# Performance work log

Measured on AMD Instinct MI355X. Metric: run time of the kernel, lower is better.

The kernel has to match this reference:

```python
import jax, jax.numpy as jnp
import numpy as np

B, T, S = 32, 64, 64
V, E, H, Hs = 32000, 512, 512, 512
D2 = 2 * Hs  # src feature dim


def setup_inputs() -> dict:
    key = jax.random.key(0)
    ks = jax.random.split(key, 26)
    n = lambda k, shape, s=0.05: (jax.random.normal(k, shape, jnp.float32) * s)
    inp = {
        'src': jax.random.normal(ks[0], (B, S, D2), jnp.float32),
        'trg': jax.random.randint(ks[1], (B, T), 0, V),
        'mask': jnp.ones((B, T), jnp.float32),
        'emb': n(ks[2], (V, E)),
        # PyTorch LSTMCell params: weight_ih [4H, E+H], weight_hh [4H, H]
        'f_Wih': n(ks[3], (4 * H, E + H)), 'f_Whh': n(ks[4], (4 * H, H)),
        'f_bih': n(ks[5], (4 * H,)), 'f_bhh': n(ks[6], (4 * H,)),
        'b_Wih': n(ks[7], (4 * H, E + H)), 'b_Whh': n(ks[8], (4 * H, H)),
        'b_bih': n(ks[9], (4 * H,)), 'b_bhh': n(ks[10], (4 * H,)),
        # attention projections: hidden -> 2*src_hidden
        'fatt_W': n(ks[11], (D2, H)), 'fatt_b': n(ks[12], (D2,)),
        'batt_W': n(ks[13], (D2, H)), 'batt_b': n(ks[14], (D2,)),
        # att_hidden linears: (H + 2*Hs) -> H
        'fah_W': n(ks[15], (H, H + D2)), 'fah_b': n(ks[16], (H,)),
        'bah_W': n(ks[17], (H, H + D2)), 'bah_b': n(ks[18], (H,)),
        # output projection 2H -> V
        'fc_W': n(ks[19], (V, 2 * H)), 'fc_b': n(ks[20], (V,)),
        'feed_init': n(ks[21], (2 * H,), 1.0),
        'hid_init': n(ks[22], (4 * H,), 1.0),
    }
    return inp


def reference(src, trg, mask, emb, f_Wih, f_Whh, f_bih, f_bhh,
              b_Wih, b_Whh, b_bih, b_bhh, fatt_W, fatt_b, batt_W, batt_b,
              fah_W, fah_b, bah_W, bah_b, fc_W, fc_b, feed_init, hid_init):
    Bn = src.shape[0]
    Hn = feed_init.shape[0] // 2
    scale = 1.0 / np.sqrt(Hn)  # key.size(-1) == trg hidden before projection

    x = emb[trg]  # [B, T, E]  (dropout p=0 -> identity)

    hhat0 = jnp.broadcast_to(feed_init, (Bn, 2 * Hn))
    f_hhat0, b_hhat0 = jnp.split(hhat0, 2, axis=1)
    hid0 = jnp.broadcast_to(hid_init, (Bn, 4 * Hn))
    f_hid, b_hid = jnp.split(hid0, 2, axis=-1)
    f_h0, f_c0 = jnp.split(f_hid, 2, axis=-1)
    b_h0, b_c0 = jnp.split(b_hid, 2, axis=-1)

    def lstm(xin, h, c, Wih, Whh, bih, bhh):
        g = xin @ Wih.T + bih + h @ Whh.T + bhh
        i, f, gg, o = jnp.split(g, 4, axis=-1)
        c = jax.nn.sigmoid(f) * c + jax.nn.sigmoid(i) * jnp.tanh(gg)
        h = jax.nn.sigmoid(o) * jnp.tanh(c)
        return h, c

    def att(h, W, b):
        k = h @ W.T + b                              # [B, 2Hs]
        w = jnp.einsum('bd,bsd->bs', k, src) * scale  # [B, S]
        p = jax.nn.softmax(w, axis=-1)
        return jnp.einsum('bs,bsd->bd', p, src)       # [B, 2Hs]

    xs = jnp.swapaxes(x, 0, 1)      # [T, B, E]
    ms = jnp.swapaxes(mask, 0, 1)   # [T, B]

    def f_step(carry, x_t):
        h, c, hhat = carry
        h, c = lstm(jnp.concatenate([x_t, hhat], -1), h, c, f_Wih, f_Whh, f_bih, f_bhh)
        ct = att(h, fatt_W, fatt_b)
        # NOTE: original uses b_att_hidden in the forward loop (faithful)
        hhat = jnp.tanh(jnp.concatenate([h, ct], -1) @ bah_W.T + bah_b)
        return (h, c, hhat), hhat

    _, f_out = jax.lax.scan(f_step, (f_h0, f_c0, f_hhat0), xs)  # [T, B, H]

    def b_step(carry, inp):
        x_t, m_t = inp
        h, c, hhat = carry
        hn, cn = lstm(jnp.concatenate([x_t, hhat], -1), h, c, b_Wih, b_Whh, b_bih, b_bhh)
        h = m_t[:, None] * hn
        c = m_t[:, None] * cn
        ct = att(h, batt_W, batt_b)
        # NOTE: original uses f_att_hidden in the backward loop (faithful)
        hhat = jnp.tanh(jnp.concatenate([h, ct], -1) @ fah_W.T + fah_b)
        return (h, c, hhat), hhat

    _, b_out = jax.lax.scan(b_step, (b_h0, b_c0, b_hhat0), (xs[::-1], ms[::-1]))

    f_out = jnp.swapaxes(f_out, 0, 1)        # [B, T, H]
    b_cheat = jnp.swapaxes(b_out, 0, 1)      # reversed-time order, as stacked in torch
    # b_outputs[:, :-2] = b_outputs_cheat[:, 2:]; last two steps zero (faithful)
    b_shift = jnp.concatenate([b_cheat[:, 2:], jnp.zeros_like(b_cheat[:, :2])], axis=1)

    logits = jnp.concatenate([f_out, b_shift], -1) @ fc_W.T + fc_b  # [B, T, V]
    return logits
```

## Files before the change

kernel.cpp:

```cpp
#include <hip/hip_runtime.h>
#include <hip/hip_bf16.h>
#include <math.h>

typedef __hip_bfloat16 bf16;
typedef __attribute__((ext_vector_type(8))) short short8b;
typedef __attribute__((ext_vector_type(8))) __bf16 bf16x8;
typedef __attribute__((ext_vector_type(4))) float f32x4;

#define SCALE_F 0.04419417382415922f

template <typename V>
static __device__ inline auto mfma_try(V a, V b, f32x4 c, int)
    -> decltype(__builtin_amdgcn_mfma_f32_16x16x32_bf16(a, b, c, 0, 0, 0)) {
  return __builtin_amdgcn_mfma_f32_16x16x32_bf16(a, b, c, 0, 0, 0);
}
template <typename V>
static __device__ inline auto mfma_try(V a, V b, f32x4 c, long)
    -> decltype(__builtin_amdgcn_mfma_f32_16x16x32_bf16(
        __builtin_bit_cast(bf16x8, a), __builtin_bit_cast(bf16x8, b), c, 0, 0, 0)) {
  return __builtin_amdgcn_mfma_f32_16x16x32_bf16(
      __builtin_bit_cast(bf16x8, a), __builtin_bit_cast(bf16x8, b), c, 0, 0, 0);
}
static __device__ inline f32x4 MFMA(short8b a, short8b b, f32x4 c) {
  return mfma_try(a, b, c, 0);
}

static __device__ inline short8b ldb8(const bf16* p) {
  return *reinterpret_cast<const short8b*>(p);
}
static __device__ inline float b2f(bf16 v) { return __bfloat162float(v); }
static __device__ inline bf16 f2b(float v) { return __float2bfloat16(v); }
static __device__ inline float s2f(short s) {
  unsigned u = ((unsigned)(unsigned short)s) << 16;
  return __builtin_bit_cast(float, u);
}
static __device__ inline float sigm(float x) { return 1.f / (1.f + expf(-x)); }

static __device__ inline void st2_wt(bf16* p, float v) {
  unsigned short u = __builtin_bit_cast(unsigned short, f2b(v));
  unsigned ud = u;
  asm volatile("global_store_short %0, %1, off sc0 sc1" ::"v"(p), "v"(ud)
               : "memory");
}

static __device__ inline void st_flag(unsigned* p, unsigned v) {
  asm volatile("global_store_dword %0, %1, off sc0 sc1" ::"v"(p), "v"(v)
               : "memory");
}
static __device__ inline unsigned ld_flag(const unsigned* p) {
  unsigned v;
  asm volatile("global_load_dword %0, %1, off sc0 sc1\n\ts_waitcnt vmcnt(0)"
               : "=v"(v)
               : "v"(p)
               : "memory");
  return v;
}

static __device__ inline void gbar(unsigned* flags, unsigned ep, int blk, int tid) {
  asm volatile("s_waitcnt vmcnt(0)" ::: "memory");
  __syncthreads();
  if (tid < 64) {
    unsigned* row = flags + (size_t)ep * 64;
    if (tid == 0) st_flag(row + blk, 1u);
    while (true) {
      const unsigned v = ld_flag(row + tid);
      if (__ballot(v != 0) == ~0ull) break;
      __builtin_amdgcn_s_sleep(1);
    }
  }
  __syncthreads();
}

template <typename OutT, bool HAS_BIAS>
__global__ __launch_bounds__(256) void gemm_k(
    const bf16* __restrict__ A, const bf16* __restrict__ Bw,
    OutT* __restrict__ C, const float* __restrict__ bias,
    int M, int N, int K) {
  const int lane = threadIdx.x & 63;
  const int wid = threadIdx.x >> 6;
  const int m0 = blockIdx.y * 128 + (wid >> 1) * 64;
  const int n0 = blockIdx.x * 128 + (wid & 1) * 64;
  const int lr = lane & 15;
  const int lk = (lane >> 4) * 8;
  f32x4 acc[4][4];
#pragma unroll
  for (int i = 0; i < 4; ++i)
#pragma unroll
    for (int j = 0; j < 4; ++j) acc[i][j] = (f32x4){0.f, 0.f, 0.f, 0.f};
  const bf16* Ap = A + (size_t)(m0 + lr) * K + lk;
  const bf16* Bp = Bw + (size_t)(n0 + lr) * K + lk;
  for (int k0 = 0; k0 < K; k0 += 32) {
    short8b av[4], bv[4];
#pragma unroll
    for (int i = 0; i < 4; ++i) av[i] = ldb8(Ap + (size_t)i * 16 * K + k0);
#pragma unroll
    for (int i = 0; i < 4; ++i) bv[i] = ldb8(Bp + (size_t)i * 16 * K + k0);
#pragma unroll
    for (int mi = 0; mi < 4; ++mi)
#pragma unroll
      for (int ni = 0; ni < 4; ++ni)
        acc[mi][ni] = MFMA(av[mi], bv[ni], acc[mi][ni]);
  }
  const int rb = (lane >> 4) * 4;
#pragma unroll
  for (int mi = 0; mi < 4; ++mi) {
#pragma unroll
    for (int r = 0; r < 4; ++r) {
      const int row = m0 + mi * 16 + rb + r;
#pragma unroll
      for (int ni = 0; ni < 4; ++ni) {
        const int col = n0 + ni * 16 + lr;
        float v = acc[mi][ni][r];
        if (HAS_BIAS) v += bias[col];
        if constexpr (sizeof(OutT) == 2) {
          C[(size_t)row * N + col] = f2b(v);
        } else {
          C[(size_t)row * N + col] = v;
        }
      }
    }
  }
}

__global__ void k_xg(const float* __restrict__ emb, const int* __restrict__ trg,
                     bf16* __restrict__ xg) {
  const int i = blockIdx.x * 256 + threadIdx.x;
  const int r = i >> 9, e = i & 511;
  const int t = r >> 5, b = r & 31;
  const int tok = trg[b * 64 + t];
  xg[i] = f2b(emb[(size_t)tok * 512 + e]);
}

__global__ void k_srcb(const float* __restrict__ s, bf16* __restrict__ d) {
  const int i = blockIdx.x * 256 + threadIdx.x;
  d[i] = f2b(s[i]);
}

__global__ void k_fcw(const float* __restrict__ s, bf16* __restrict__ d) {
  const size_t stride = (size_t)gridDim.x * blockDim.x;
  for (size_t i = blockIdx.x * (size_t)blockDim.x + threadIdx.x;
       i < (size_t)32000 * 1024; i += stride)
    d[i] = f2b(s[i]);
}

__global__ void k_wpack(const float* __restrict__ fWih, const float* __restrict__ fWhh,
                        const float* __restrict__ bWih, const float* __restrict__ bWhh,
                        const float* __restrict__ fattW, const float* __restrict__ battW,
                        const float* __restrict__ bahW, const float* __restrict__ fahW,
                        bf16* Wxf, bf16* Wxb, bf16* Wrecf, bf16* Wrecb,
                        bf16* attWtf, bf16* attWtb, bf16* ahW2f, bf16* ahW2b,
                        bf16* Wh1f, bf16* Wh1b) {
  const int stride = gridDim.x * blockDim.x;
  const int i0 = blockIdx.x * blockDim.x + threadIdx.x;
  for (int i = i0; i < 2048 * 512; i += stride) {
    const int gc = i >> 9, k = i & 511;
    Wxf[i] = f2b(fWih[(size_t)gc * 1024 + k]);
    Wxb[i] = f2b(bWih[(size_t)gc * 1024 + k]);
  }
  for (int i = i0; i < 2048 * 1024; i += stride) {
    const int gc = i >> 10, k = i & 1023;
    float vf, vb;
    if (k < 512) { vf = fWih[(size_t)gc * 1024 + 512 + k]; vb = bWih[(size_t)gc * 1024 + 512 + k]; }
    else         { vf = fWhh[(size_t)gc * 512 + k - 512]; vb = bWhh[(size_t)gc * 512 + k - 512]; }
    Wrecf[i] = f2b(vf); Wrecb[i] = f2b(vb);
  }
  for (int i = i0; i < 512 * 1024; i += stride) {
    const int j = i >> 10, d = i & 1023;
    attWtf[i] = f2b(fattW[(size_t)d * 512 + j]);
    attWtb[i] = f2b(battW[(size_t)d * 512 + j]);
  }
  for (int i = i0; i < 512 * 1024; i += stride) {
    const int o = i >> 10, d = i & 1023;
    ahW2f[i] = f2b(bahW[(size_t)o * 1536 + 512 + d]);
    ahW2b[i] = f2b(fahW[(size_t)o * 1536 + 512 + d]);
  }
  for (int i = i0; i < 512 * 512; i += stride) {
    const int o = i >> 9, k = i & 511;
    Wh1f[i] = f2b(bahW[(size_t)o * 1536 + k]);
    Wh1b[i] = f2b(fahW[(size_t)o * 1536 + k]);
  }
}

__global__ void k_c0(const float* __restrict__ src, const float* __restrict__ fb,
                     const float* __restrict__ bb, float* __restrict__ c0f,
                     float* __restrict__ c0b) {
  const int r = blockIdx.x;
  const int tid = threadIdx.x;
  float pf = 0.f, pb = 0.f;
  for (int d = tid; d < 1024; d += 256) {
    const float s = src[(size_t)r * 1024 + d];
    pf += s * fb[d];
    pb += s * bb[d];
  }
#pragma unroll
  for (int d = 1; d < 64; d <<= 1) { pf += __shfl_xor(pf, d); pb += __shfl_xor(pb, d); }
  __shared__ float rf[4], rb2[4];
  if ((tid & 63) == 0) { rf[tid >> 6] = pf; rb2[tid >> 6] = pb; }
  __syncthreads();
  if (tid == 0) {
    c0f[r] = (rf[0] + rf[1] + rf[2] + rf[3]) * SCALE_F;
    c0b[r] = (rb2[0] + rb2[1] + rb2[2] + rb2[3]) * SCALE_F;
  }
}

__global__ void k_init(const float* __restrict__ feed, const float* __restrict__ hid,
                       bf16* hh0, bf16* hh1, bf16* hb0, bf16* hb1,
                       float* cst0, float* cst1) {
  const int i = blockIdx.x * 256 + threadIdx.x;
  const int b = i >> 9, k = i & 511;
  hh0[i] = f2b(feed[k]);
  hh1[i] = f2b(feed[512 + k]);
  hb0[i] = f2b(hid[k]);
  hb1[i] = f2b(hid[1024 + k]);
  cst0[k * 32 + b] = hid[512 + k];
  cst1[k * 32 + b] = hid[1536 + k];
}

struct ScanP {
  const bf16* Wrec[2]; const bf16* Xp[2]; const bf16* Af[2]; const bf16* Bm[2];
  const bf16* Wh1[2]; const float* bih[2]; const float* bhh[2];
  const float* c0[2]; const float* ahb[2]; const float* mask;
  bf16* hh[2]; bf16* hb[2]; bf16* U[2]; float* cst[2]; bf16* hcat; unsigned* flags;
};

__global__ __launch_bounds__(256) void scan_k(ScanP P) {
  const int blk = blockIdx.x;
  const int dir = blk >> 5;
  const int g = blk & 31;
  const int tid = threadIdx.x;
  const int lane = tid & 63;
  const int wv = tid >> 6;

  const bf16* __restrict__ Wrec = P.Wrec[dir];
  const bf16* __restrict__ Xp = P.Xp[dir];
  const bf16* __restrict__ Af = P.Af[dir];
  const bf16* __restrict__ Bm = P.Bm[dir];
  const bf16* __restrict__ Wh1 = P.Wh1[dir];
  const float* __restrict__ bihp = P.bih[dir];
  const float* __restrict__ bhhp = P.bhh[dir];
  const float* __restrict__ c0v = P.c0[dir];
  const float* __restrict__ ahbp = P.ahb[dir];
  bf16* __restrict__ hhB = P.hh[dir];
  bf16* __restrict__ hbB = P.hb[dir];
  bf16* __restrict__ Ubuf = P.U[dir];
  float* __restrict__ cst = P.cst[dir];

  __shared__ float gl[4][16][33];
  __shared__ float h_lds[512];
  __shared__ float w_part[2][64];
  __shared__ float p_lds[64];

  unsigned ep = 0;
  const int lr16 = lane & 15;
  const int koff = (lane >> 4) * 8;

  short8b pA0[16], pA1[16];
  {
    const bf16* A0 = hbB + (size_t)lr16 * 512;
    const bf16* A1 = hbB + (size_t)(lr16 + 16) * 512;
#pragma unroll
    for (int ks = 0; ks < 16; ++ks) {
      pA0[ks] = ldb8(A0 + ks * 32 + koff);
      pA1[ks] = ldb8(A1 + ks * 32 + koff);
    }
  }

  for (int t = 0; t < 64; ++t) {
    const bf16* hhR = hhB + (size_t)t * 32 * 512;
    bf16* hhW = hhB + (size_t)(t + 1) * 32 * 512;
    bf16* hbW = hbB + (size_t)(t + 1) * 32 * 512;

    {
      const int gate = wv;
      const int gc = gate * 512 + g * 16 + lr16;
      const bf16* Brow = Wrec + (size_t)gc * 1024;
      const bf16* A0h = hhR + (size_t)lr16 * 512;
      const bf16* A1h = hhR + (size_t)(lr16 + 16) * 512;
      f32x4 ac0 = (f32x4){0.f, 0.f, 0.f, 0.f};
      f32x4 ac1 = (f32x4){0.f, 0.f, 0.f, 0.f};
#pragma unroll
      for (int ks = 0; ks < 16; ++ks) {
        const int k = ks * 32 + koff;
        const short8b bv = ldb8(Brow + 512 + k);
        ac0 = MFMA(pA0[ks], bv, ac0);
        ac1 = MFMA(pA1[ks], bv, ac1);
      }
#pragma unroll
      for (int ks = 0; ks < 16; ++ks) {
        const int k = ks * 32 + koff;
        const short8b bv = ldb8(Brow + k);
        ac0 = MFMA(ldb8(A0h + k), bv, ac0);
        ac1 = MFMA(ldb8(A1h + k), bv, ac1);
      }
      const int tcol = dir ? (63 - t) : t;
      const float bsum = bihp[gc] + bhhp[gc];
      const bf16* xpc = Xp + (size_t)gc * 2048 + tcol * 32;
#pragma unroll
      for (int r = 0; r < 4; ++r) {
        const int brow = (lane >> 4) * 4 + r;
        gl[gate][lr16][brow] = ac0[r] + b2f(xpc[brow]) + bsum;
        gl[gate][lr16][brow + 16] = ac1[r] + b2f(xpc[brow + 16]) + bsum;
      }
    }
    __syncthreads();
    {
      const int b = tid & 31;
#pragma unroll
      for (int it = 0; it < 2; ++it) {
        const int jl = (tid >> 5) + it * 8;
        const int j = g * 16 + jl;
        const float gi = gl[0][jl][b];
        const float gf = gl[1][jl][b];
        const float gg = gl[2][jl][b];
        const float go = gl[3][jl][b];
        float cn = sigm(gf) * cst[j * 32 + b] + sigm(gi) * tanhf(gg);
        float hn = sigm(go) * tanhf(cn);
        if (dir) {
          const float m = P.mask[b * 64 + (63 - t)];
          hn *= m; cn *= m;
        }
        cst[j * 32 + b] = cn;
        st2_wt(hbW + (size_t)b * 512 + j, hn);
      }
    }
    gbar(P.flags, ep++, blk, tid);

    if (wv == 0) {
      const bf16* Brow = Wh1 + (size_t)(g * 16 + lr16) * 512;
      const bf16* A0 = hbW + (size_t)lr16 * 512;
      const bf16* A1 = hbW + (size_t)(lr16 + 16) * 512;
      f32x4 u0 = (f32x4){0.f, 0.f, 0.f, 0.f};
      f32x4 u1 = (f32x4){0.f, 0.f, 0.f, 0.f};
#pragma unroll
      for (int ks = 0; ks < 16; ++ks) {
        const int k = ks * 32 + koff;
        const short8b bv = ldb8(Brow + k);
        u0 = MFMA(ldb8(A0 + k), bv, u0);
        u1 = MFMA(ldb8(A1 + k), bv, u1);
      }
      bf16* Uw = Ubuf + (size_t)t * 32 * 512;
      const int o = g * 16 + lr16;
#pragma unroll
      for (int r = 0; r < 4; ++r) {
        const int b0 = (lane >> 4) * 4 + r;
        st2_wt(Uw + (size_t)b0 * 512 + o, u0[r]);
        st2_wt(Uw + (size_t)(b0 + 16) * 512 + o, u1[r]);
      }
    } else if (wv == 1) {
      const short8b v = ldb8(hbW + (size_t)g * 512 + lane * 8);
#pragma unroll
      for (int e = 0; e < 8; ++e) h_lds[lane * 8 + e] = s2f(v[e]);
    }
    __syncthreads();
    if (wv == 1 || wv == 2) {
      const int s = lane, q = wv - 1;
      const bf16* arow = Af + (size_t)(g * 64 + s) * 512 + q * 256;
      float part = 0.f;
#pragma unroll 4
      for (int k8 = 0; k8 < 256; k8 += 8) {
        const short8b v = ldb8(arow + k8);
#pragma unroll
        for (int e = 0; e < 8; ++e) part += h_lds[q * 256 + k8 + e] * s2f(v[e]);
      }
      w_part[q][s] = part;
    }
    __syncthreads();
    if (wv == 3) {
      const float v = (w_part[0][lane] + w_part[1][lane]) * SCALE_F + c0v[g * 64 + lane];
      float mx = v;
#pragma unroll
      for (int d = 1; d < 64; d <<= 1) mx = fmaxf(mx, __shfl_xor(mx, d));
      const float e = expf(v - mx);
      float sm = e;
#pragma unroll
      for (int d = 1; d < 64; d <<= 1) sm += __shfl_xor(sm, d);
      p_lds[lane] = e / sm;
    }
    __syncthreads();
    float a2[2];
#pragma unroll
    for (int it = 0; it < 2; ++it) {
      const int o = tid + it * 256;
      float acc = ahbp[o];
      const bf16* bmc = Bm + (size_t)(g * 64) * 512 + o;
#pragma unroll 4
      for (int s2 = 0; s2 < 64; ++s2) acc += p_lds[s2] * b2f(bmc[(size_t)s2 * 512]);
      a2[it] = acc;
    }
    gbar(P.flags, ep++, blk, tid);

    {
      const bf16* Ur = Ubuf + ((size_t)t * 32 + g) * 512;
#pragma unroll
      for (int it = 0; it < 2; ++it) {
        const int o = tid + it * 256;
        const float hh = tanhf(a2[it] + b2f(Ur[o]));
        st2_wt(hhW + (size_t)g * 512 + o, hh);
        if (dir == 0) {
          P.hcat[(size_t)(g * 64 + t) * 1024 + o] = f2b(hh);
        } else if (t >= 2) {
          P.hcat[(size_t)(g * 64 + t - 2) * 1024 + 512 + o] = f2b(hh);
        }
      }
      if (t < 63) {
        const bf16* A0 = hbW + (size_t)lr16 * 512;
        const bf16* A1 = hbW + (size_t)(lr16 + 16) * 512;
#pragma unroll
        for (int ks = 0; ks < 16; ++ks) {
          pA0[ks] = ldb8(A0 + ks * 32 + koff);
          pA1[ks] = ldb8(A1 + ks * 32 + koff);
        }
      }
    }
    gbar(P.flags, ep++, blk, tid);
  }
}

extern "C" void kernel_launch(void* const* d_in, const int* in_sizes, int n_in,
                              void* d_out, int out_size, void* d_ws, size_t ws_size,
                              hipStream_t stream) {
  (void)in_sizes; (void)n_in; (void)out_size; (void)ws_size;
  const float* src  = (const float*)d_in[0];
  const int*   trg  = (const int*)d_in[1];
  const float* mask = (const float*)d_in[2];
  const float* emb  = (const float*)d_in[3];
  const float* fWih = (const float*)d_in[4];
  const float* fWhh = (const float*)d_in[5];
  const float* fbih = (const float*)d_in[6];
  const float* fbhh = (const float*)d_in[7];
  const float* bWih = (const float*)d_in[8];
  const float* bWhh = (const float*)d_in[9];
  const float* bbih = (const float*)d_in[10];
  const float* bbhh = (const float*)d_in[11];
  const float* fattW = (const float*)d_in[12];
  const float* fattb = (const float*)d_in[13];
  const float* battW = (const float*)d_in[14];
  const float* battb = (const float*)d_in[15];
  const float* fahW = (const float*)d_in[16];
  const float* fahb = (const float*)d_in[17];
  const float* bahW = (const float*)d_in[18];
  const float* bahb = (const float*)d_in[19];
  const float* fcW  = (const float*)d_in[20];
  const float* fcb  = (const float*)d_in[21];
  const float* feed = (const float*)d_in[22];
  const float* hid  = (const float*)d_in[23];

  char* wsp = (char*)d_ws;
  size_t off = 0;
  auto alloc = [&](size_t bytes) -> void* {
    void* p = wsp + off;
    off += (bytes + 255) & ~(size_t)255;
    return p;
  };
  unsigned* flags = (unsigned*)alloc((size_t)192 * 64 * 4);
  bf16* hcat = (bf16*)alloc((size_t)2048 * 1024 * 2);
  const size_t zero_bytes = off;
  bf16* xg    = (bf16*)alloc((size_t)2048 * 512 * 2);
  bf16* srcb  = (bf16*)alloc((size_t)2048 * 1024 * 2);
  bf16* fcWb  = (bf16*)alloc((size_t)32000 * 1024 * 2);
  bf16* Wxf   = (bf16*)alloc((size_t)2048 * 512 * 2);
  bf16* Wxb   = (bf16*)alloc((size_t)2048 * 512 * 2);
  bf16* Wrecf = (bf16*)alloc((size_t)2048 * 1024 * 2);
  bf16* Wrecb = (bf16*)alloc((size_t)2048 * 1024 * 2);
  bf16* attWtf = (bf16*)alloc((size_t)512 * 1024 * 2);
  bf16* attWtb = (bf16*)alloc((size_t)512 * 1024 * 2);
  bf16* ahW2f = (bf16*)alloc((size_t)512 * 1024 * 2);
  bf16* ahW2b = (bf16*)alloc((size_t)512 * 1024 * 2);
  bf16* Wh1f  = (bf16*)alloc((size_t)512 * 512 * 2);
  bf16* Wh1b  = (bf16*)alloc((size_t)512 * 512 * 2);
  bf16* Xpf   = (bf16*)alloc((size_t)2048 * 2048 * 2);
  bf16* Xpb   = (bf16*)alloc((size_t)2048 * 2048 * 2);
  bf16* Aff   = (bf16*)alloc((size_t)2048 * 512 * 2);
  bf16* Afb   = (bf16*)alloc((size_t)2048 * 512 * 2);
  bf16* Bmf   = (bf16*)alloc((size_t)2048 * 512 * 2);
  bf16* Bmb   = (bf16*)alloc((size_t)2048 * 512 * 2);
  float* c0f  = (float*)alloc(2048 * 4);
  float* c0b  = (float*)alloc(2048 * 4);
  bf16* hh0   = (bf16*)alloc((size_t)65 * 32 * 512 * 2);
  bf16* hh1   = (bf16*)alloc((size_t)65 * 32 * 512 * 2);
  bf16* hb0   = (bf16*)alloc((size_t)65 * 32 * 512 * 2);
  bf16* hb1   = (bf16*)alloc((size_t)65 * 32 * 512 * 2);
  bf16* Uf    = (bf16*)alloc((size_t)64 * 32 * 512 * 2);
  bf16* Ub    = (bf16*)alloc((size_t)64 * 32 * 512 * 2);
  float* cst0 = (float*)alloc((size_t)512 * 32 * 4);
  float* cst1 = (float*)alloc((size_t)512 * 32 * 4);

  hipMemsetAsync(d_ws, 0, zero_bytes, stream);

  k_xg<<<4096, 256, 0, stream>>>(emb, trg, xg);
  k_srcb<<<8192, 256, 0, stream>>>(src, srcb);
  k_fcw<<<8192, 256, 0, stream>>>(fcW, fcWb);
  k_wpack<<<2048, 256, 0, stream>>>(fWih, fWhh, bWih, bWhh, fattW, battW, bahW, fahW,
                                    Wxf, Wxb, Wrecf, Wrecb, attWtf, attWtb, ahW2f, ahW2b,
                                    Wh1f, Wh1b);
  k_c0<<<2048, 256, 0, stream>>>(src, fattb, battb, c0f, c0b);
  k_init<<<64, 256, 0, stream>>>(feed, hid, hh0, hh1, hb0, hb1, cst0, cst1);

  gemm_k<bf16, false><<<dim3(16, 16), 256, 0, stream>>>(Wxf, xg, Xpf, nullptr, 2048, 2048, 512);
  gemm_k<bf16, false><<<dim3(16, 16), 256, 0, stream>>>(Wxb, xg, Xpb, nullptr, 2048, 2048, 512);
  gemm_k<bf16, false><<<dim3(4, 16), 256, 0, stream>>>(srcb, attWtf, Aff, nullptr, 2048, 512, 1024);
  gemm_k<bf16, false><<<dim3(4, 16), 256, 0, stream>>>(srcb, attWtb, Afb, nullptr, 2048, 512, 1024);
  gemm_k<bf16, false><<<dim3(4, 16), 256, 0, stream>>>(srcb, ahW2f, Bmf, nullptr, 2048, 512, 1024);
  gemm_k<bf16, false><<<dim3(4, 16), 256, 0, stream>>>(srcb, ahW2b, Bmb, nullptr, 2048, 512, 1024);

  ScanP sp;
  sp.Wrec[0] = Wrecf; sp.Wrec[1] = Wrecb;
  sp.Xp[0] = Xpf;     sp.Xp[1] = Xpb;
  sp.Af[0] = Aff;     sp.Af[1] = Afb;
  sp.Bm[0] = Bmf;     sp.Bm[1] = Bmb;
  sp.Wh1[0] = Wh1f;   sp.Wh1[1] = Wh1b;
  sp.bih[0] = fbih;   sp.bih[1] = bbih;
  sp.bhh[0] = fbhh;   sp.bhh[1] = bbhh;
  sp.c0[0] = c0f;     sp.c0[1] = c0b;
  sp.ahb[0] = bahb;   sp.ahb[1] = fahb;
  sp.mask = mask;
  sp.hh[0] = hh0;     sp.hh[1] = hh1;
  sp.hb[0] = hb0;     sp.hb[1] = hb1;
  sp.U[0] = Uf;       sp.U[1] = Ub;
  sp.cst[0] = cst0;   sp.cst[1] = cst1;
  sp.hcat = hcat;     sp.flags = flags;
  scan_k<<<64, 256, 0, stream>>>(sp);

  gemm_k<float, true><<<dim3(250, 16), 256, 0, stream>>>(hcat, fcWb, (float*)d_out, fcb,
                                                         2048, 32000, 1024);
}
```

Before: 2.940 ms.

## Consolidate scan into 16 large blocks with per-direction 8-block grid barriers

The recurrent scan kernel now runs as 16 blocks of 1024 threads, each packing four former 256-thread groups, instead of 64 blocks of 256. Grid barriers are split per direction and wait on only 8 flags, which cuts the number of participants in each cross-block sync. The kernel also drops the register-cached hb operand in favour of reloading it each step, and it packs bf16 stores into dword writes. The trade-off is fewer CUs doing the per-step work and more register and LDS pressure per block.

```diff
diff --git a/kernel.cpp b/kernel.cpp
--- a/kernel.cpp
+++ b/kernel.cpp
@@ -34,12 +34,21 @@
   unsigned u = ((unsigned)(unsigned short)s) << 16;
   return __builtin_bit_cast(float, u);
 }
+static __device__ inline unsigned pack2(float lo, float hi) {
+  const unsigned a = (unsigned)__builtin_bit_cast(unsigned short, f2b(lo));
+  const unsigned b = (unsigned)__builtin_bit_cast(unsigned short, f2b(hi));
+  return a | (b << 16);
+}
 static __device__ inline float sigm(float x) { return 1.f / (1.f + expf(-x)); }
 
 static __device__ inline void st2_wt(bf16* p, float v) {
-  unsigned short u = __builtin_bit_cast(unsigned short, f2b(v));
-  unsigned ud = u;
+  unsigned ud = (unsigned)__builtin_bit_cast(unsigned short, f2b(v));
   asm volatile("global_store_short %0, %1, off sc0 sc1" ::"v"(p), "v"(ud)
+               : "memory");
+}
+static __device__ inline void st4_wt(bf16* p, float lo, float hi) {
+  unsigned ud = pack2(lo, hi);
+  asm volatile("global_store_dword %0, %1, off sc0 sc1" ::"v"(p), "v"(ud)
                : "memory");
 }
 
@@ -56,14 +65,14 @@
   return v;
 }
 
-static __device__ inline void gbar(unsigned* flags, unsigned ep, int blk, int tid) {
+static __device__ inline void gbar8(unsigned* flg, unsigned ep, int bd, int tid) {
   asm volatile("s_waitcnt vmcnt(0)" ::: "memory");
   __syncthreads();
   if (tid < 64) {
-    unsigned* row = flags + (size_t)ep * 64;
-    if (tid == 0) st_flag(row + blk, 1u);
+    unsigned* row = flg + (size_t)ep * 64;
+    if (tid == 0) st_flag(row + bd, 1u);
     while (true) {
-      const unsigned v = ld_flag(row + tid);
+      const unsigned v = ld_flag(row + (tid & 7));
       if (__ballot(v != 0) == ~0ull) break;
       __builtin_amdgcn_s_sleep(1);
     }
@@ -223,13 +232,15 @@
   bf16* hh[2]; bf16* hb[2]; bf16* U[2]; float* cst[2]; bf16* hcat; unsigned* flags;
 };
 
-__global__ __launch_bounds__(256) void scan_k(ScanP P) {
+__global__ __launch_bounds__(1024) void scan_k(ScanP P) {
   const int blk = blockIdx.x;
-  const int dir = blk >> 5;
-  const int g = blk & 31;
+  const int dir = blk >> 3;
+  const int bd = blk & 7;
   const int tid = threadIdx.x;
   const int lane = tid & 63;
   const int wv = tid >> 6;
+  const int grp = wv >> 2;
+  const int sub = wv & 3;
 
   const bf16* __restrict__ Wrec = P.Wrec[dir];
   const bf16* __restrict__ Xp = P.Xp[dir];
@@ -244,88 +255,81 @@
   bf16* __restrict__ hbB = P.hb[dir];
   bf16* __restrict__ Ubuf = P.U[dir];
   float* __restrict__ cst = P.cst[dir];
-
-  __shared__ float gl[4][16][33];
-  __shared__ float h_lds[512];
-  __shared__ float w_part[2][64];
-  __shared__ float p_lds[64];
+  unsigned* __restrict__ flg = P.flags + (size_t)dir * 192 * 64;
+
+  __shared__ float gl[4][4][16][33];
+  __shared__ float h_lds[4][512];
+  __shared__ float w_part[4][2][64];
+  __shared__ float p_lds[4][64];
 
   unsigned ep = 0;
   const int lr16 = lane & 15;
-  const int koff = (lane >> 4) * 8;
-
-  short8b pA0[16], pA1[16];
-  {
-    const bf16* A0 = hbB + (size_t)lr16 * 512;
-    const bf16* A1 = hbB + (size_t)(lr16 + 16) * 512;
-#pragma unroll
-    for (int ks = 0; ks < 16; ++ks) {
-      pA0[ks] = ldb8(A0 + ks * 32 + koff);
-      pA1[ks] = ldb8(A1 + ks * 32 + koff);
-    }
-  }
+  const int kb = lane >> 4;
+  const int koff = kb * 8;
+  const int g = bd * 4 + grp;
 
   for (int t = 0; t < 64; ++t) {
     const bf16* hhR = hhB + (size_t)t * 32 * 512;
     bf16* hhW = hhB + (size_t)(t + 1) * 32 * 512;
+    const bf16* hbR = hbB + (size_t)t * 32 * 512;
     bf16* hbW = hbB + (size_t)(t + 1) * 32 * 512;
 
     {
-      const int gate = wv;
+      const int gate = sub;
       const int gc = gate * 512 + g * 16 + lr16;
       const bf16* Brow = Wrec + (size_t)gc * 1024;
       const bf16* A0h = hhR + (size_t)lr16 * 512;
       const bf16* A1h = hhR + (size_t)(lr16 + 16) * 512;
+      const bf16* A0g = hbR + (size_t)lr16 * 512;
+      const bf16* A1g = hbR + (size_t)(lr16 + 16) * 512;
       f32x4 ac0 = (f32x4){0.f, 0.f, 0.f, 0.f};
       f32x4 ac1 = (f32x4){0.f, 0.f, 0.f, 0.f};
 #pragma unroll
       for (int ks = 0; ks < 16; ++ks) {
         const int k = ks * 32 + koff;
-        const short8b bv = ldb8(Brow + 512 + k);
-        ac0 = MFMA(pA0[ks], bv, ac0);
-        ac1 = MFMA(pA1[ks], bv, ac1);
-      }
-#pragma unroll
-      for (int ks = 0; ks < 16; ++ks) {
-        const int k = ks * 32 + koff;
-        const short8b bv = ldb8(Brow + k);
-        ac0 = MFMA(ldb8(A0h + k), bv, ac0);
-        ac1 = MFMA(ldb8(A1h + k), bv, ac1);
+        const short8b bh = ldb8(Brow + 512 + k);
+        ac0 = MFMA(ldb8(A0g + k), bh, ac0);
+        ac1 = MFMA(ldb8(A1g + k), bh, ac1);
+        const short8b bx = ldb8(Brow + k);
+        ac0 = MFMA(ldb8(A0h + k), bx, ac0);
+        ac1 = MFMA(ldb8(A1h + k), bx, ac1);
       }
       const int tcol = dir ? (63 - t) : t;
       const float bsum = bihp[gc] + bhhp[gc];
       const bf16* xpc = Xp + (size_t)gc * 2048 + tcol * 32;
 #pragma unroll
       for (int r = 0; r < 4; ++r) {
-        const int brow = (lane >> 4) * 4 + r;
-        gl[gate][lr16][brow] = ac0[r] + b2f(xpc[brow]) + bsum;
-        gl[gate][lr16][brow + 16] = ac1[r] + b2f(xpc[brow + 16]) + bsum;
+        const int brow = kb * 4 + r;
+        gl[gate][grp][lr16][brow] = ac0[r] + b2f(xpc[brow]) + bsum;
+        gl[gate][grp][lr16][brow + 16] = ac1[r] + b2f(xpc[brow + 16]) + bsum;
       }
     }
     __syncthreads();
     {
-      const int b = tid & 31;
-#pragma unroll
-      for (int it = 0; it < 2; ++it) {
-        const int jl = (tid >> 5) + it * 8;
-        const int j = g * 16 + jl;
-        const float gi = gl[0][jl][b];
-        const float gf = gl[1][jl][b];
-        const float gg = gl[2][jl][b];
-        const float go = gl[3][jl][b];
+      const int b = tid >> 5;
+      const int j2 = tid & 31;
+      const float m = dir ? P.mask[b * 64 + (63 - t)] : 1.f;
+      float hn2[2];
+#pragma unroll
+      for (int u = 0; u < 2; ++u) {
+        const int jl = j2 * 2 + u;
+        const int jq = jl >> 4, jr = jl & 15;
+        const float gi = gl[0][jq][jr][b];
+        const float gf = gl[1][jq][jr][b];
+        const float gg = gl[2][jq][jr][b];
+        const float go = gl[3][jq][jr][b];
+        const int j = bd * 64 + jl;
         float cn = sigm(gf) * cst[j * 32 + b] + sigm(gi) * tanhf(gg);
         float hn = sigm(go) * tanhf(cn);
-        if (dir) {
-          const float m = P.mask[b * 64 + (63 - t)];
-          hn *= m; cn *= m;
-        }
+        hn *= m; cn *= m;
         cst[j * 32 + b] = cn;
-        st2_wt(hbW + (size_t)b * 512 + j, hn);
-      }
-    }
-    gbar(P.flags, ep++, blk, tid);
-
-    if (wv == 0) {
+        hn2[u] = hn;
+      }
+      st4_wt(hbW + (size_t)b * 512 + bd * 64 + j2 * 2, hn2[0], hn2[1]);
+    }
+    gbar8(flg, ep++, bd, tid);
+
+    if (sub == 0) {
       const bf16* Brow = Wh1 + (size_t)(g * 16 + lr16) * 512;
       const bf16* A0 = hbW + (size_t)lr16 * 512;
       const bf16* A1 = hbW + (size_t)(lr16 + 16) * 512;
@@ -342,31 +346,32 @@
       const int o = g * 16 + lr16;
 #pragma unroll
       for (int r = 0; r < 4; ++r) {
-        const int b0 = (lane >> 4) * 4 + r;
+        const int b0 = kb * 4 + r;
         st2_wt(Uw + (size_t)b0 * 512 + o, u0[r]);
         st2_wt(Uw + (size_t)(b0 + 16) * 512 + o, u1[r]);
       }
-    } else if (wv == 1) {
+    } else if (sub == 1) {
       const short8b v = ldb8(hbW + (size_t)g * 512 + lane * 8);
 #pragma unroll
-      for (int e = 0; e < 8; ++e) h_lds[lane * 8 + e] = s2f(v[e]);
+      for (int e = 0; e < 8; ++e) h_lds[grp][lane * 8 + e] = s2f(v[e]);
     }
     __syncthreads();
-    if (wv == 1 || wv == 2) {
-      const int s = lane, q = wv - 1;
-      const bf16* arow = Af + (size_t)(g * 64 + s) * 512 + q * 256;
+    if (sub == 1 || sub == 2) {
+      const int q = sub - 1;
+      const bf16* arow = Af + (size_t)(g * 64 + lane) * 512 + q * 256;
       float part = 0.f;
 #pragma unroll 4
       for (int k8 = 0; k8 < 256; k8 += 8) {
         const short8b v = ldb8(arow + k8);
 #pragma unroll
-        for (int e = 0; e < 8; ++e) part += h_lds[q * 256 + k8 + e] * s2f(v[e]);
-      }
-      w_part[q][s] = part;
+        for (int e = 0; e < 8; ++e) part += h_lds[grp][q * 256 + k8 + e] * s2f(v[e]);
+      }
+      w_part[grp][q][lane] = part;
     }
     __syncthreads();
-    if (wv == 3) {
-      const float v = (w_part[0][lane] + w_part[1][lane]) * SCALE_F + c0v[g * 64 + lane];
+    if (sub == 3) {
+      const float v = (w_part[grp][0][lane] + w_part[grp][1][lane]) * SCALE_F +
+                      c0v[g * 64 + lane];
       float mx = v;
 #pragma unroll
       for (int d = 1; d < 64; d <<= 1) mx = fmaxf(mx, __shfl_xor(mx, d));
@@ -374,45 +379,42 @@
       float sm = e;
 #pragma unroll
       for (int d = 1; d < 64; d <<= 1) sm += __shfl_xor(sm, d);
-      p_lds[lane] = e / sm;
+      p_lds[grp][lane] = e / sm;
     }
     __syncthreads();
     float a2[2];
-#pragma unroll
-    for (int it = 0; it < 2; ++it) {
-      const int o = tid + it * 256;
-      float acc = ahbp[o];
-      const bf16* bmc = Bm + (size_t)(g * 64) * 512 + o;
+    {
+      const int tg = sub * 64 + lane;
+      const int o2 = tg * 2;
+      a2[0] = ahbp[o2];
+      a2[1] = ahbp[o2 + 1];
+      const bf16* bmc = Bm + (size_t)(g * 64) * 512 + o2;
 #pragma unroll 4
-      for (int s2 = 0; s2 < 64; ++s2) acc += p_lds[s2] * b2f(bmc[(size_t)s2 * 512]);
-      a2[it] = acc;
-    }
-    gbar(P.flags, ep++, blk, tid);
+      for (int s2 = 0; s2 < 64; ++s2) {
+        const unsigned uv = *reinterpret_cast<const unsigned*>(bmc + (size_t)s2 * 512);
+        const float p = p_lds[grp][s2];
+        a2[0] += p * s2f((short)(uv & 0xffffu));
+        a2[1] += p * s2f((short)(uv >> 16));
+      }
+    }
+    gbar8(flg, ep++, bd, tid);
 
     {
-      const bf16* Ur = Ubuf + ((size_t)t * 32 + g) * 512;
-#pragma unroll
-      for (int it = 0; it < 2; ++it) {
-        const int o = tid + it * 256;
-        const float hh = tanhf(a2[it] + b2f(Ur[o]));
-        st2_wt(hhW + (size_t)g * 512 + o, hh);
-        if (dir == 0) {
-          P.hcat[(size_t)(g * 64 + t) * 1024 + o] = f2b(hh);
-        } else if (t >= 2) {
-          P.hcat[(size_t)(g * 64 + t - 2) * 1024 + 512 + o] = f2b(hh);
-        }
-      }
-      if (t < 63) {
-        const bf16* A0 = hbW + (size_t)lr16 * 512;
-        const bf16* A1 = hbW + (size_t)(lr16 + 16) * 512;
-#pragma unroll
-        for (int ks = 0; ks < 16; ++ks) {
-          pA0[ks] = ldb8(A0 + ks * 32 + koff);
-          pA1[ks] = ldb8(A1 + ks * 32 + koff);
-        }
-      }
-    }
-    gbar(P.flags, ep++, blk, tid);
+      const int tg = sub * 64 + lane;
+      const int o2 = tg * 2;
+      const unsigned uu =
+          *reinterpret_cast<const unsigned*>(Ubuf + ((size_t)t * 32 + g) * 512 + o2);
+      const float h0 = tanhf(a2[0] + s2f((short)(uu & 0xffffu)));
+      const float h1 = tanhf(a2[1] + s2f((short)(uu >> 16)));
+      st4_wt(hhW + (size_t)g * 512 + o2, h0, h1);
+      const unsigned hp = pack2(h0, h1);
+      if (dir == 0) {
+        *reinterpret_cast<unsigned*>(P.hcat + (size_t)(g * 64 + t) * 1024 + o2) = hp;
+      } else if (t >= 2) {
+        *reinterpret_cast<unsigned*>(P.hcat + (size_t)(g * 64 + t - 2) * 1024 + 512 + o2) = hp;
+      }
+    }
+    gbar8(flg, ep++, bd, tid);
   }
 }
 
@@ -452,7 +454,7 @@
     off += (bytes + 255) & ~(size_t)255;
     return p;
   };
-  unsigned* flags = (unsigned*)alloc((size_t)192 * 64 * 4);
+  unsigned* flags = (unsigned*)alloc((size_t)2 * 192 * 64 * 4);
   bf16* hcat = (bf16*)alloc((size_t)2048 * 1024 * 2);
   const size_t zero_bytes = off;
   bf16* xg    = (bf16*)alloc((size_t)2048 * 512 * 2);
@@ -519,7 +521,7 @@
   sp.U[0] = Uf;       sp.U[1] = Ub;
   sp.cst[0] = cst0;   sp.cst[1] = cst1;
   sp.hcat = hcat;     sp.flags = flags;
-  scan_k<<<64, 256, 0, stream>>>(sp);
+  scan_k<<<16, 1024, 0, stream>>>(sp);
 
   gemm_k<float, true><<<dim3(250, 16), 256, 0, stream>>>(hcat, fcWb, (float*)d_out, fcb,
                                                          2048, 32000, 1024);
```

Result: slower. 5.093 ms (+73.2%).

## Pin each scan direction to one XCC and use per-direction barriers

Applied to the files above, without the earlier changes.

The scan kernel now launches many blocks and reads the hardware XCC id. Blocks on XCC 0 and 1 claim ranks through atomics, so each direction's 32 workgroups share one XCC and its L2, and all other blocks exit. The global barrier is split per direction over 32 groups, and the write-through sc0/sc1 stores of the shared h/U buffers become plain stores, relying on same-XCC L2 coherence. This targets cross-XCC synchronisation and coherence cost in the recurrent loop, but it depends on the hardware dispatching enough blocks to each XCC, adds a bounded spin guard that can fall through silently, and it adds a tiny launch of many exiting blocks.

```diff
diff --git a/kernel.cpp b/kernel.cpp
--- a/kernel.cpp
+++ b/kernel.cpp
@@ -34,13 +34,16 @@
   unsigned u = ((unsigned)(unsigned short)s) << 16;
   return __builtin_bit_cast(float, u);
 }
+static __device__ inline unsigned pack2(float lo, float hi) {
+  const unsigned a = (unsigned)__builtin_bit_cast(unsigned short, f2b(lo));
+  const unsigned b = (unsigned)__builtin_bit_cast(unsigned short, f2b(hi));
+  return a | (b << 16);
+}
 static __device__ inline float sigm(float x) { return 1.f / (1.f + expf(-x)); }
 
-static __device__ inline void st2_wt(bf16* p, float v) {
-  unsigned short u = __builtin_bit_cast(unsigned short, f2b(v));
-  unsigned ud = u;
-  asm volatile("global_store_short %0, %1, off sc0 sc1" ::"v"(p), "v"(ud)
-               : "memory");
+static __device__ inline void st2p(bf16* p, float v) { *p = f2b(v); }
+static __device__ inline void st4p(bf16* p, float lo, float hi) {
+  *reinterpret_cast<unsigned*>(p) = pack2(lo, hi);
 }
 
 static __device__ inline void st_flag(unsigned* p, unsigned v) {
@@ -56,14 +59,15 @@
   return v;
 }
 
-static __device__ inline void gbar(unsigned* flags, unsigned ep, int blk, int tid) {
+static __device__ inline void xbar(unsigned* flg, unsigned ep, int g, int tid) {
   asm volatile("s_waitcnt vmcnt(0)" ::: "memory");
   __syncthreads();
   if (tid < 64) {
-    unsigned* row = flags + (size_t)ep * 64;
-    if (tid == 0) st_flag(row + blk, 1u);
-    while (true) {
-      const unsigned v = ld_flag(row + tid);
+    unsigned* row = flg + (size_t)ep * 64;
+    if (tid == 0) st_flag(row + g, 1u);
+    int guard = 0;
+    while (guard++ < (1 << 22)) {
+      const unsigned v = ld_flag(row + (tid & 31));
       if (__ballot(v != 0) == ~0ull) break;
       __builtin_amdgcn_s_sleep(1);
     }
@@ -220,13 +224,26 @@
   const bf16* Wrec[2]; const bf16* Xp[2]; const bf16* Af[2]; const bf16* Bm[2];
   const bf16* Wh1[2]; const float* bih[2]; const float* bhh[2];
   const float* c0[2]; const float* ahb[2]; const float* mask;
-  bf16* hh[2]; bf16* hb[2]; bf16* U[2]; float* cst[2]; bf16* hcat; unsigned* flags;
+  bf16* hh[2]; bf16* hb[2]; bf16* U[2]; float* cst[2]; bf16* hcat;
+  unsigned* flags; unsigned* claim;
 };
 
 __global__ __launch_bounds__(256) void scan_k(ScanP P) {
-  const int blk = blockIdx.x;
-  const int dir = blk >> 5;
-  const int g = blk & 31;
+  __shared__ int s_dir, s_g;
+  if (threadIdx.x == 0) {
+    unsigned xcc;
+    asm volatile("s_getreg_b32 %0, hwreg(HW_REG_XCC_ID)" : "=s"(xcc));
+    xcc &= 7u;
+    int rank = 1000;
+    if (xcc < 2) rank = (int)atomicAdd(P.claim + xcc, 1u);
+    s_dir = (int)xcc;
+    s_g = rank;
+  }
+  __syncthreads();
+  const int dir = s_dir;
+  const int g = s_g;
+  if (dir >= 2 || g >= 32) return;
+
   const int tid = threadIdx.x;
   const int lane = tid & 63;
   const int wv = tid >> 6;
@@ -244,6 +261,7 @@
   bf16* __restrict__ hbB = P.hb[dir];
   bf16* __restrict__ Ubuf = P.U[dir];
   float* __restrict__ cst = P.cst[dir];
+  unsigned* __restrict__ flg = P.flags + (size_t)dir * 192 * 64;
 
   __shared__ float gl[4][16][33];
   __shared__ float h_lds[512];
@@ -252,7 +270,8 @@
 
   unsigned ep = 0;
   const int lr16 = lane & 15;
-  const int koff = (lane >> 4) * 8;
+  const int kb = lane >> 4;
+  const int koff = kb * 8;
 
   short8b pA0[16], pA1[16];
   {
@@ -297,7 +316,7 @@
       const bf16* xpc = Xp + (size_t)gc * 2048 + tcol * 32;
 #pragma unroll
       for (int r = 0; r < 4; ++r) {
-        const int brow = (lane >> 4) * 4 + r;
+        const int brow = kb * 4 + r;
         gl[gate][lr16][brow] = ac0[r] + b2f(xpc[brow]) + bsum;
         gl[gate][lr16][brow + 16] = ac1[r] + b2f(xpc[brow + 16]) + bsum;
       }
@@ -320,10 +339,10 @@
           hn *= m; cn *= m;
         }
         cst[j * 32 + b] = cn;
-        st2_wt(hbW + (size_t)b * 512 + j, hn);
-      }
-    }
-    gbar(P.flags, ep++, blk, tid);
+        st2p(hbW + (size_t)b * 512 + j, hn);
+      }
+    }
+    xbar(flg, ep++, g, tid);
 
     if (wv == 0) {
       const bf16* Brow = Wh1 + (size_t)(g * 16 + lr16) * 512;
@@ -342,9 +361,9 @@
       const int o = g * 16 + lr16;
 #pragma unroll
       for (int r = 0; r < 4; ++r) {
-        const int b0 = (lane >> 4) * 4 + r;
-        st2_wt(Uw + (size_t)b0 * 512 + o, u0[r]);
-        st2_wt(Uw + (size_t)(b0 + 16) * 512 + o, u1[r]);
+        const int b0 = kb * 4 + r;
+        st2p(Uw + (size_t)b0 * 512 + o, u0[r]);
+        st2p(Uw + (size_t)(b0 + 16) * 512 + o, u1[r]);
       }
     } else if (wv == 1) {
       const short8b v = ldb8(hbW + (size_t)g * 512 + lane * 8);
@@ -353,8 +372,8 @@
     }
     __syncthreads();
     if (wv == 1 || wv == 2) {
-      const int s = lane, q = wv - 1;
-      const bf16* arow = Af + (size_t)(g * 64 + s) * 512 + q * 256;
+      const int q = wv - 1;
+      const bf16* arow = Af + (size_t)(g * 64 + lane) * 512 + q * 256;
       float part = 0.f;
 #pragma unroll 4
       for (int k8 = 0; k8 < 256; k8 += 8) {
@@ -362,7 +381,7 @@
 #pragma unroll
         for (int e = 0; e < 8; ++e) part += h_lds[q * 256 + k8 + e] * s2f(v[e]);
       }
-      w_part[q][s] = part;
+      w_part[q][lane] = part;
     }
     __syncthreads();
     if (wv == 3) {
@@ -387,7 +406,7 @@
       for (int s2 = 0; s2 < 64; ++s2) acc += p_lds[s2] * b2f(bmc[(size_t)s2 * 512]);
       a2[it] = acc;
     }
-    gbar(P.flags, ep++, blk, tid);
+    xbar(flg, ep++, g, tid);
 
     {
       const bf16* Ur = Ubuf + ((size_t)t * 32 + g) * 512;
@@ -395,7 +414,7 @@
       for (int it = 0; it < 2; ++it) {
         const int o = tid + it * 256;
         const float hh = tanhf(a2[it] + b2f(Ur[o]));
-        st2_wt(hhW + (size_t)g * 512 + o, hh);
+        st2p(hhW + (size_t)g * 512 + o, hh);
         if (dir == 0) {
           P.hcat[(size_t)(g * 64 + t) * 1024 + o] = f2b(hh);
         } else if (t >= 2) {
@@ -412,7 +431,7 @@
         }
       }
     }
-    gbar(P.flags, ep++, blk, tid);
+    xbar(flg, ep++, g, tid);
   }
 }
 
@@ -452,7 +471,8 @@
     off += (bytes + 255) & ~(size_t)255;
     return p;
   };
-  unsigned* flags = (unsigned*)alloc((size_t)192 * 64 * 4);
+  unsigned* claim = (unsigned*)alloc(64);
+  unsigned* flags = (unsigned*)alloc((size_t)2 * 192 * 64 * 4);
   bf16* hcat = (bf16*)alloc((size_t)2048 * 1024 * 2);
   const size_t zero_bytes = off;
   bf16* xg    = (bf16*)alloc((size_t)2048 * 512 * 2);
@@ -518,8 +538,8 @@
   sp.hb[0] = hb0;     sp.hb[1] = hb1;
   sp.U[0] = Uf;       sp.U[1] = Ub;
   sp.cst[0] = cst0;   sp.cst[1] = cst1;
-  sp.hcat = hcat;     sp.flags = flags;
-  scan_k<<<64, 256, 0, stream>>>(sp);
+  sp.hcat = hcat;     sp.flags = flags;    sp.claim = claim;
+  scan_k<<<1024, 256, 0, stream>>>(sp);
 
   gemm_k<float, true><<<dim3(250, 16), 256, 0, stream>>>(hcat, fcWb, (float*)d_out, fcb,
                                                          2048, 32000, 1024);
```

Result: no change. 2.892 ms (-1.6%).

## Transpose attention-hidden matrix and vectorize loads/stores in recurrent scan

Applied to the files above, without the earlier changes.

Adds a pre-scan transpose of the Bm attention-hidden products so each thread reads contiguous 64-element rows with 16-byte loads, replacing strided scalar loads in the per-step context reduction. It also packs pairs of bf16 outputs into dword stores for h, hhat and hcat, and batches the A-operand loads of the recurrent MFMA loop ahead of use. The aim is to cut memory latency and instruction count on the latency-bound sequential scan. The cost is an extra transpose kernel, extra workspace, and higher register pressure from the batched loads.

```diff
diff --git a/kernel.cpp b/kernel.cpp
--- a/kernel.cpp
+++ b/kernel.cpp
@@ -34,12 +34,21 @@
   unsigned u = ((unsigned)(unsigned short)s) << 16;
   return __builtin_bit_cast(float, u);
 }
+static __device__ inline unsigned pack2(float lo, float hi) {
+  const unsigned a = (unsigned)__builtin_bit_cast(unsigned short, f2b(lo));
+  const unsigned b = (unsigned)__builtin_bit_cast(unsigned short, f2b(hi));
+  return a | (b << 16);
+}
 static __device__ inline float sigm(float x) { return 1.f / (1.f + expf(-x)); }
 
 static __device__ inline void st2_wt(bf16* p, float v) {
-  unsigned short u = __builtin_bit_cast(unsigned short, f2b(v));
-  unsigned ud = u;
+  unsigned ud = (unsigned)__builtin_bit_cast(unsigned short, f2b(v));
   asm volatile("global_store_short %0, %1, off sc0 sc1" ::"v"(p), "v"(ud)
+               : "memory");
+}
+static __device__ inline void st4_wt(bf16* p, float lo, float hi) {
+  unsigned ud = pack2(lo, hi);
+  asm volatile("global_store_dword %0, %1, off sc0 sc1" ::"v"(p), "v"(ud)
                : "memory");
 }
 
@@ -141,6 +150,12 @@
   for (size_t i = blockIdx.x * (size_t)blockDim.x + threadIdx.x;
        i < (size_t)32000 * 1024; i += stride)
     d[i] = f2b(s[i]);
+}
+
+__global__ void k_bmt(const bf16* __restrict__ in, bf16* __restrict__ out) {
+  const int i = blockIdx.x * 256 + threadIdx.x;
+  const int b = i >> 15, rem = i & 32767, o = rem >> 6, s = rem & 63;
+  out[i] = in[(size_t)(b * 64 + s) * 512 + o];
 }
 
 __global__ void k_wpack(const float* __restrict__ fWih, const float* __restrict__ fWhh,
@@ -217,7 +232,7 @@
 }
 
 struct ScanP {
-  const bf16* Wrec[2]; const bf16* Xp[2]; const bf16* Af[2]; const bf16* Bm[2];
+  const bf16* Wrec[2]; const bf16* Xp[2]; const bf16* Af[2]; const bf16* Bmt[2];
   const bf16* Wh1[2]; const float* bih[2]; const float* bhh[2];
   const float* c0[2]; const float* ahb[2]; const float* mask;
   bf16* hh[2]; bf16* hb[2]; bf16* U[2]; float* cst[2]; bf16* hcat; unsigned* flags;
@@ -234,7 +249,7 @@
   const bf16* __restrict__ Wrec = P.Wrec[dir];
   const bf16* __restrict__ Xp = P.Xp[dir];
   const bf16* __restrict__ Af = P.Af[dir];
-  const bf16* __restrict__ Bm = P.Bm[dir];
+  const bf16* __restrict__ Bmt = P.Bmt[dir];
   const bf16* __restrict__ Wh1 = P.Wh1[dir];
   const float* __restrict__ bihp = P.bih[dir];
   const float* __restrict__ bhhp = P.bhh[dir];
@@ -252,7 +267,8 @@
 
   unsigned ep = 0;
   const int lr16 = lane & 15;
-  const int koff = (lane >> 4) * 8;
+  const int kb = lane >> 4;
+  const int koff = kb * 8;
 
   short8b pA0[16], pA1[16];
   {
@@ -286,18 +302,28 @@
         ac1 = MFMA(pA1[ks], bv, ac1);
       }
 #pragma unroll
-      for (int ks = 0; ks < 16; ++ks) {
-        const int k = ks * 32 + koff;
-        const short8b bv = ldb8(Brow + k);
-        ac0 = MFMA(ldb8(A0h + k), bv, ac0);
-        ac1 = MFMA(ldb8(A1h + k), bv, ac1);
+      for (int c = 0; c < 2; ++c) {
+        short8b sa[8], sb[8];
+#pragma unroll
+        for (int i = 0; i < 8; ++i) {
+          const int k = (c * 8 + i) * 32 + koff;
+          sa[i] = ldb8(A0h + k);
+          sb[i] = ldb8(A1h + k);
+        }
+#pragma unroll
+        for (int i = 0; i < 8; ++i) {
+          const int k = (c * 8 + i) * 32 + koff;
+          const short8b bv = ldb8(Brow + k);
+          ac0 = MFMA(sa[i], bv, ac0);
+          ac1 = MFMA(sb[i], bv, ac1);
+        }
       }
       const int tcol = dir ? (63 - t) : t;
       const float bsum = bihp[gc] + bhhp[gc];
       const bf16* xpc = Xp + (size_t)gc * 2048 + tcol * 32;
 #pragma unroll
       for (int r = 0; r < 4; ++r) {
-        const int brow = (lane >> 4) * 4 + r;
+        const int brow = kb * 4 + r;
         gl[gate][lr16][brow] = ac0[r] + b2f(xpc[brow]) + bsum;
         gl[gate][lr16][brow + 16] = ac1[r] + b2f(xpc[brow + 16]) + bsum;
       }
@@ -305,9 +331,11 @@
     __syncthreads();
     {
       const int b = tid & 31;
-#pragma unroll
-      for (int it = 0; it < 2; ++it) {
-        const int jl = (tid >> 5) + it * 8;
+      const int jp = (tid >> 5) * 2;
+      float hn2[2];
+#pragma unroll
+      for (int u = 0; u < 2; ++u) {
+        const int jl = jp + u;
         const int j = g * 16 + jl;
         const float gi = gl[0][jl][b];
         const float gf = gl[1][jl][b];
@@ -320,8 +348,9 @@
           hn *= m; cn *= m;
         }
         cst[j * 32 + b] = cn;
-        st2_wt(hbW + (size_t)b * 512 + j, hn);
-      }
+        hn2[u] = hn;
+      }
+      st4_wt(hbW + (size_t)b * 512 + g * 16 + jp, hn2[0], hn2[1]);
     }
     gbar(P.flags, ep++, blk, tid);
 
@@ -342,7 +371,7 @@
       const int o = g * 16 + lr16;
 #pragma unroll
       for (int r = 0; r < 4; ++r) {
-        const int b0 = (lane >> 4) * 4 + r;
+        const int b0 = kb * 4 + r;
         st2_wt(Uw + (size_t)b0 * 512 + o, u0[r]);
         st2_wt(Uw + (size_t)(b0 + 16) * 512 + o, u1[r]);
       }
@@ -353,16 +382,16 @@
     }
     __syncthreads();
     if (wv == 1 || wv == 2) {
-      const int s = lane, q = wv - 1;
-      const bf16* arow = Af + (size_t)(g * 64 + s) * 512 + q * 256;
+      const int q = wv - 1;
+      const bf16* arow = Af + (size_t)(g * 64 + lane) * 512 + q * 256;
       float part = 0.f;
-#pragma unroll 4
+#pragma unroll 8
       for (int k8 = 0; k8 < 256; k8 += 8) {
         const short8b v = ldb8(arow + k8);
 #pragma unroll
         for (int e = 0; e < 8; ++e) part += h_lds[q * 256 + k8 + e] * s2f(v[e]);
       }
-      w_part[q][s] = part;
+      w_part[q][lane] = part;
     }
     __syncthreads();
     if (wv == 3) {
@@ -378,29 +407,40 @@
     }
     __syncthreads();
     float a2[2];
-#pragma unroll
-    for (int it = 0; it < 2; ++it) {
-      const int o = tid + it * 256;
-      float acc = ahbp[o];
-      const bf16* bmc = Bm + (size_t)(g * 64) * 512 + o;
-#pragma unroll 4
-      for (int s2 = 0; s2 < 64; ++s2) acc += p_lds[s2] * b2f(bmc[(size_t)s2 * 512]);
-      a2[it] = acc;
+    {
+      const int o2 = tid * 2;
+      const bf16* bm0 = Bmt + ((size_t)g * 512 + o2) * 64;
+      short8b v0[8], v1[8];
+#pragma unroll
+      for (int i = 0; i < 8; ++i) {
+        v0[i] = ldb8(bm0 + i * 8);
+        v1[i] = ldb8(bm0 + 64 + i * 8);
+      }
+      float s0 = ahbp[o2], s1 = ahbp[o2 + 1];
+#pragma unroll
+      for (int i = 0; i < 8; ++i)
+#pragma unroll
+        for (int e = 0; e < 8; ++e) {
+          const float p = p_lds[i * 8 + e];
+          s0 += p * s2f(v0[i][e]);
+          s1 += p * s2f(v1[i][e]);
+        }
+      a2[0] = s0; a2[1] = s1;
     }
     gbar(P.flags, ep++, blk, tid);
 
     {
-      const bf16* Ur = Ubuf + ((size_t)t * 32 + g) * 512;
-#pragma unroll
-      for (int it = 0; it < 2; ++it) {
-        const int o = tid + it * 256;
-        const float hh = tanhf(a2[it] + b2f(Ur[o]));
-        st2_wt(hhW + (size_t)g * 512 + o, hh);
-        if (dir == 0) {
-          P.hcat[(size_t)(g * 64 + t) * 1024 + o] = f2b(hh);
-        } else if (t >= 2) {
-          P.hcat[(size_t)(g * 64 + t - 2) * 1024 + 512 + o] = f2b(hh);
-        }
+      const int o2 = tid * 2;
+      const unsigned uu =
+          *reinterpret_cast<const unsigned*>(Ubuf + ((size_t)t * 32 + g) * 512 + o2);
+      const float h0 = tanhf(a2[0] + s2f((short)(uu & 0xffffu)));
+      const float h1 = tanhf(a2[1] + s2f((short)(uu >> 16)));
+      st4_wt(hhW + (size_t)g * 512 + o2, h0, h1);
+      const unsigned hp = pack2(h0, h1);
+      if (dir == 0) {
+        *reinterpret_cast<unsigned*>(P.hcat + (size_t)(g * 64 + t) * 1024 + o2) = hp;
+      } else if (t >= 2) {
+        *reinterpret_cast<unsigned*>(P.hcat + (size_t)(g * 64 + t - 2) * 1024 + 512 + o2) = hp;
       }
       if (t < 63) {
         const bf16* A0 = hbW + (size_t)lr16 * 512;
@@ -474,6 +514,8 @@
   bf16* Afb   = (bf16*)alloc((size_t)2048 * 512 * 2);
   bf16* Bmf   = (bf16*)alloc((size_t)2048 * 512 * 2);
   bf16* Bmb   = (bf16*)alloc((size_t)2048 * 512 * 2);
+  bf16* Bmtf  = (bf16*)alloc((size_t)2048 * 512 * 2);
+  bf16* Bmtb  = (bf16*)alloc((size_t)2048 * 512 * 2);
   float* c0f  = (float*)alloc(2048 * 4);
   float* c0b  = (float*)alloc(2048 * 4);
   bf16* hh0   = (bf16*)alloc((size_t)65 * 32 * 512 * 2);
@@ -502,12 +544,14 @@
   gemm_k<bf16, false><<<dim3(4, 16), 256, 0, stream>>>(srcb, attWtb, Afb, nullptr, 2048, 512, 1024);
   gemm_k<bf16, false><<<dim3(4, 16), 256, 0, stream>>>(srcb, ahW2f, Bmf, nullptr, 2048, 512, 1024);
   gemm_k<bf16, false><<<dim3(4, 16), 256, 0, stream>>>(srcb, ahW2b, Bmb, nullptr, 2048, 512, 1024);
+  k_bmt<<<4096, 256, 0, stream>>>(Bmf, Bmtf);
+  k_bmt<<<4096, 256, 0, stream>>>(Bmb, Bmtb);
 
   ScanP sp;
   sp.Wrec[0] = Wrecf; sp.Wrec[1] = Wrecb;
   sp.Xp[0] = Xpf;     sp.Xp[1] = Xpb;
   sp.Af[0] = Aff;     sp.Af[1] = Afb;
-  sp.Bm[0] = Bmf;     sp.Bm[1] = Bmb;
+  sp.Bmt[0] = Bmtf;   sp.Bmt[1] = Bmtb;
   sp.Wh1[0] = Wh1f;   sp.Wh1[1] = Wh1b;
   sp.bih[0] = fbih;   sp.bih[1] = bbih;
   sp.bhh[0] = fbhh;   sp.bhh[1] = bbhh;
```

Result: faster. 2.867 ms (-2.5%).
